# Kernel optimization log

Measured on AMD Instinct MI355X. Metric: run time of the kernel, lower is better.

## Reference

```python
import jax, jax.numpy as jnp
import numpy as np

N = 8192
H = 512
TAU = 0.8
LAM = 0.5
EPS = 1e-8


def setup_inputs() -> dict:
    key = jax.random.key(0)
    k1, k2, k3, k4, k5 = jax.random.split(key, 5)
    xavier_std = 1.414 * np.sqrt(2.0 / (H + H))  # xavier_normal_ with gain=1.414
    return {
        "z_mp": jax.random.normal(k1, (N, H), dtype=jnp.float32),
        "z_sc": jax.random.normal(k2, (N, H), dtype=jnp.float32),
        "pos": jax.random.randint(k3, (N, N), 0, 2, dtype=jnp.int32),
        "W1": (jax.random.normal(k4, (H, H), dtype=jnp.float32) * xavier_std),
        "b1": jnp.zeros((H,), dtype=jnp.float32),
        "W2": (jax.random.normal(k5, (H, H), dtype=jnp.float32) * xavier_std),
        "b2": jnp.zeros((H,), dtype=jnp.float32),
    }


def _proj(z, W1, b1, W2, b2):
    # nn.Linear applies x @ W.T + b
    h = jax.nn.elu(z @ W1.T + b1)
    return h @ W2.T + b2


def _sim(z1, z2, tau):
    # exp(cosine_similarity / tau), computed as in the original:
    # dot(z1, z2.T) / (|z1| |z2|.T) / tau
    n1 = jnp.linalg.norm(z1, axis=-1, keepdims=True)  # [N,1]
    n2 = jnp.linalg.norm(z2, axis=-1, keepdims=True)  # [N,1]
    dot = z1 @ z2.T                                   # [N,N]
    return jnp.exp(dot / (n1 * n2.T) / tau)


def reference(z_mp, z_sc, pos, W1, b1, W2, b2):
    pos_f = pos.astype(jnp.float32)
    zp_mp = _proj(z_mp, W1, b1, W2, b2)
    zp_sc = _proj(z_sc, W1, b1, W2, b2)

    m_mp2sc = _sim(zp_mp, zp_sc, TAU)   # [N,N]
    m_sc2mp = m_mp2sc.T                 # [N,N]

    # row-normalize, masked log-mean (mp -> sc)
    s_mp = m_mp2sc / (jnp.sum(m_mp2sc, axis=1, keepdims=True) + EPS)
    lori_mp = -jnp.mean(jnp.log(jnp.sum(s_mp * pos_f, axis=-1)))

    # row-normalize, masked log-mean (sc -> mp)
    s_sc = m_sc2mp / (jnp.sum(m_sc2mp, axis=1, keepdims=True) + EPS)
    lori_sc = -jnp.mean(jnp.log(jnp.sum(s_sc * pos_f, axis=-1)))

    return LAM * lori_mp + (1.0 - LAM) * lori_sc
```

## Files before the change

kernel.cpp:

```cpp
#include <hip/hip_runtime.h>
#include <stdint.h>


#define NN 8192
#define HH 512
#define TAUF 0.8f
#define EPSF 1e-8f
#define NW (NN / 32)

typedef __attribute__((ext_vector_type(8))) short short8;
typedef __attribute__((ext_vector_type(4))) float f32x4;
typedef __attribute__((ext_vector_type(4))) int i32x4;
typedef __attribute__((ext_vector_type(4))) unsigned short u16x4;
typedef unsigned short u16;
typedef unsigned int u32;

typedef __attribute__((address_space(1))) void GV;
typedef __attribute__((address_space(3))) void LV;

__device__ __forceinline__ void g2l16(const void* g, void* l) {
  __builtin_amdgcn_global_load_lds((const GV*)g, (LV*)l, 16, 0, 0);
}

__device__ __forceinline__ u16 f2bf(float x) {
  u32 u = __builtin_bit_cast(u32, x);
  u = (u + 0x7fffu + ((u >> 16) & 1u)) >> 16;
  return (u16)u;
}

__global__ __launch_bounds__(256)
void pack_kernel(const int* __restrict__ pos, u32* __restrict__ P) {
  int gid = blockIdx.x * 256 + threadIdx.x;
  const int* src = pos + (size_t)gid * 32;
  u32 w = 0;
#pragma unroll
  for (int c = 0; c < 8; ++c) {
    i32x4 p = *(const i32x4*)(src + c * 4);
    w |= ((u32)p.x & 1u) << (c * 4);
    w |= ((u32)p.y & 1u) << (c * 4 + 1);
    w |= ((u32)p.z & 1u) << (c * 4 + 2);
    w |= ((u32)p.w & 1u) << (c * 4 + 3);
  }
  P[gid] = w;
}

__global__ void cast_kernel(const float* __restrict__ in, u16* __restrict__ out, int n) {
  int i = (blockIdx.x * 256 + threadIdx.x) * 8;
  if (i >= n) return;
  f32x4 a = *(const f32x4*)(in + i);
  f32x4 b = *(const f32x4*)(in + i + 4);
  u16 o[8];
  o[0] = f2bf(a.x); o[1] = f2bf(a.y); o[2] = f2bf(a.z); o[3] = f2bf(a.w);
  o[4] = f2bf(b.x); o[5] = f2bf(b.y); o[6] = f2bf(b.z); o[7] = f2bf(b.w);
  i32x4 v;
  v.x = (int)(o[0] | ((u32)o[1] << 16)); v.y = (int)(o[2] | ((u32)o[3] << 16));
  v.z = (int)(o[4] | ((u32)o[5] << 16)); v.w = (int)(o[6] | ((u32)o[7] << 16));
  *(i32x4*)(out + i) = v;
}

template <int EPI>
__global__ __launch_bounds__(256)
void gemm_proj(const u16* __restrict__ A1, const u16* __restrict__ A2,
               const u16* __restrict__ W, const float* __restrict__ bias,
               void* __restrict__ out1, void* __restrict__ out2) {
  __shared__ __align__(16) u16 As[128 * 32];
  __shared__ __align__(16) u16 Bs[128 * 32];
  const int tid = threadIdx.x;
  const int lane = tid & 63, w = tid >> 6;
  const int lo = lane & 15, quad = lane >> 4;
  const int wy = w >> 1, wx = w & 1;
  const u16* A; char* Out; int m0;
  if (blockIdx.y < 64) { A = A1; Out = (char*)out1; m0 = blockIdx.y * 128; }
  else                 { A = A2; Out = (char*)out2; m0 = (blockIdx.y - 64) * 128; }
  const int n0 = blockIdx.x * 128;
  const int srow = w * 16 + (lane >> 2);
  const int skel = (lane & 3) * 8;
  char* AsB = (char*)As; char* BsB = (char*)Bs;
  f32x4 acc[4][4] = {};

  for (int k0 = 0; k0 < HH; k0 += 32) {
    const u16* ga = A + (size_t)(m0 + srow) * HH + k0 + skel;
    const u16* gb = W + (size_t)(n0 + srow) * HH + k0 + skel;
    g2l16(ga, AsB + w * 1024);
    g2l16(ga + (size_t)64 * HH, AsB + w * 1024 + 4096);
    g2l16(gb, BsB + w * 1024);
    g2l16(gb + (size_t)64 * HH, BsB + w * 1024 + 4096);
    asm volatile("s_waitcnt vmcnt(0)" ::: "memory");
    __syncthreads();
    short8 aF[4], bF[4];
#pragma unroll
    for (int mi = 0; mi < 4; ++mi)
      aF[mi] = *(const short8*)(AsB + (wy * 64 + mi * 16 + lo) * 64 + quad * 16);
#pragma unroll
    for (int ni = 0; ni < 4; ++ni)
      bF[ni] = *(const short8*)(BsB + (wx * 64 + ni * 16 + lo) * 64 + quad * 16);
#pragma unroll
    for (int mi = 0; mi < 4; ++mi)
#pragma unroll
      for (int ni = 0; ni < 4; ++ni)
        acc[mi][ni] = __builtin_amdgcn_mfma_f32_16x16x32_bf16(aF[mi], bF[ni], acc[mi][ni], 0, 0, 0);
    __syncthreads();
  }
#pragma unroll
  for (int mi = 0; mi < 4; ++mi) {
    int rl = wy * 64 + mi * 16 + quad * 4;
#pragma unroll
    for (int ni = 0; ni < 4; ++ni) {
      int cl = wx * 64 + ni * 16 + lo;
      float bv = bias[n0 + cl];
#pragma unroll
      for (int r = 0; r < 4; ++r) {
        float v = acc[mi][ni][r] + bv;
        size_t idx = (size_t)(m0 + rl + r) * HH + (n0 + cl);
        if (EPI == 0) {
          if (v < 0.f) v = __expf(v) - 1.f;
          ((u16*)Out)[idx] = f2bf(v);
        } else {
          ((float*)Out)[idx] = v;
        }
      }
    }
  }
}

__global__ void norm_kernel(const float* __restrict__ zp, u16* __restrict__ out, float scale) {
  const int row = blockIdx.x;
  const int t = threadIdx.x;
  const float* src = zp + (size_t)row * HH;
  f32x4 v = *(const f32x4*)(src + t * 4);
  float ss = v.x * v.x + v.y * v.y + v.z * v.z + v.w * v.w;
#pragma unroll
  for (int d = 1; d < 64; d <<= 1) ss += __shfl_xor(ss, d, 64);
  __shared__ float red[2];
  if ((t & 63) == 0) red[t >> 6] = ss;
  __syncthreads();
  float inv = scale * rsqrtf(red[0] + red[1]);
  u16x4 o;
  o[0] = f2bf(v.x * inv); o[1] = f2bf(v.y * inv);
  o[2] = f2bf(v.z * inv); o[3] = f2bf(v.w * inv);
  *(u16x4*)(out + (size_t)row * HH + t * 4) = o;
}

__global__ __launch_bounds__(256)
void sim_kernel(const u16* __restrict__ Az, const u16* __restrict__ Bz,
                const u32* __restrict__ Pbits,
                float* __restrict__ rowpart, float* __restrict__ posrowpart,
                float* __restrict__ colpart, float* __restrict__ poscolpart) {
  __shared__ __align__(16) u16 As[128 * 32];
  __shared__ __align__(16) u16 Bs[128 * 32];
  __shared__ u32 PBi[128 * 4];
  __shared__ u32 PBj[128 * 4];
  const int tid = threadIdx.x;
  const int lane = tid & 63, w = tid >> 6;
  const int lo = lane & 15, quad = lane >> 4;
  const int wy = w >> 1, wx = w & 1;

  const int bid = blockIdx.x + (int)gridDim.x * blockIdx.y;
  const int xcd = bid & 7, s = bid >> 3;
  const int by = xcd * 8 + (s >> 6);
  const int bx = s & 63;
  const int i0 = by * 128, j0 = bx * 128;

  const int srow = w * 16 + (lane >> 2);
  const int skel = (lane & 3) * 8;
  char* AsB = (char*)As; char* BsB = (char*)Bs;
  f32x4 acc[4][4] = {};

  for (int k0 = 0; k0 < HH; k0 += 32) {
    const u16* ga = Az + (size_t)(i0 + srow) * HH + k0 + skel;
    const u16* gb = Bz + (size_t)(j0 + srow) * HH + k0 + skel;
    g2l16(ga, AsB + w * 1024);
    g2l16(ga + (size_t)64 * HH, AsB + w * 1024 + 4096);
    g2l16(gb, BsB + w * 1024);
    g2l16(gb + (size_t)64 * HH, BsB + w * 1024 + 4096);
    asm volatile("s_waitcnt vmcnt(0)" ::: "memory");
    __syncthreads();
    short8 aF[4], bF[4];
#pragma unroll
    for (int mi = 0; mi < 4; ++mi)
      aF[mi] = *(const short8*)(AsB + (wy * 64 + mi * 16 + lo) * 64 + quad * 16);
#pragma unroll
    for (int ni = 0; ni < 4; ++ni)
      bF[ni] = *(const short8*)(BsB + (wx * 64 + ni * 16 + lo) * 64 + quad * 16);
#pragma unroll
    for (int mi = 0; mi < 4; ++mi)
#pragma unroll
      for (int ni = 0; ni < 4; ++ni)
        acc[mi][ni] = __builtin_amdgcn_mfma_f32_16x16x32_bf16(aF[mi], bF[ni], acc[mi][ni], 0, 0, 0);
    __syncthreads();
  }

  {
    int il = tid >> 1, w2 = (tid & 1) * 2;
    u32 a0 = Pbits[(size_t)(i0 + il) * NW + (j0 >> 5) + w2];
    u32 a1 = Pbits[(size_t)(i0 + il) * NW + (j0 >> 5) + w2 + 1];
    u32 b0 = Pbits[(size_t)(j0 + il) * NW + (i0 >> 5) + w2];
    u32 b1 = Pbits[(size_t)(j0 + il) * NW + (i0 >> 5) + w2 + 1];
    PBi[il * 4 + w2] = a0; PBi[il * 4 + w2 + 1] = a1;
    PBj[il * 4 + w2] = b0; PBj[il * 4 + w2 + 1] = b1;
  }

#pragma unroll
  for (int mi = 0; mi < 4; ++mi)
#pragma unroll
    for (int ni = 0; ni < 4; ++ni)
#pragma unroll
      for (int r = 0; r < 4; ++r)
        acc[mi][ni][r] = __expf(acc[mi][ni][r]);

  __syncthreads();

  const int rowb = wy * 64 + quad * 4;
  const int colb = wx * 64 + lo;

#pragma unroll
  for (int mi = 0; mi < 4; ++mi) {
    int rl = rowb + mi * 16;
    float rs[4], pr[4];
#pragma unroll
    for (int r = 0; r < 4; ++r) {
      u32 W0 = PBi[(rl + r) * 4 + wx * 2];
      u32 W1 = PBi[(rl + r) * 4 + wx * 2 + 1];
      float e0 = acc[mi][0][r], e1 = acc[mi][1][r];
      float e2 = acc[mi][2][r], e3 = acc[mi][3][r];
      rs[r] = (e0 + e1) + (e2 + e3);
      pr[r] = (((W0 >> lo) & 1u) ? e0 : 0.f) + (((W0 >> (16 + lo)) & 1u) ? e1 : 0.f) +
              (((W1 >> lo) & 1u) ? e2 : 0.f) + (((W1 >> (16 + lo)) & 1u) ? e3 : 0.f);
    }
#pragma unroll
    for (int d = 1; d < 16; d <<= 1) {
#pragma unroll
      for (int r = 0; r < 4; ++r) {
        rs[r] += __shfl_xor(rs[r], d, 64);
        pr[r] += __shfl_xor(pr[r], d, 64);
      }
    }
    if (lo == 0) {
      float* rp = rowpart + (size_t)(bx * 2 + wx) * NN;
      float* pp = posrowpart + (size_t)(bx * 2 + wx) * NN;
#pragma unroll
      for (int r = 0; r < 4; ++r) {
        rp[i0 + rl + r] = rs[r];
        pp[i0 + rl + r] = pr[r];
      }
    }
  }

#pragma unroll
  for (int ni = 0; ni < 4; ++ni) {
    int cl = colb + ni * 16;
    u32 W0 = PBj[cl * 4 + wy * 2];
    u32 W1 = PBj[cl * 4 + wy * 2 + 1];
    float cs = 0.f, pc = 0.f;
#pragma unroll
    for (int mi = 0; mi < 4; ++mi) {
      u32 W = (mi < 2) ? W0 : W1;
      int sh = (mi & 1) * 16 + quad * 4;
#pragma unroll
      for (int r = 0; r < 4; ++r) {
        float e = acc[mi][ni][r];
        cs += e;
        pc += ((W >> (sh + r)) & 1u) ? e : 0.f;
      }
    }
    cs += __shfl_xor(cs, 16, 64); cs += __shfl_xor(cs, 32, 64);
    pc += __shfl_xor(pc, 16, 64); pc += __shfl_xor(pc, 32, 64);
    if (quad == 0) {
      colpart[(size_t)(by * 2 + wy) * NN + j0 + cl] = cs;
      poscolpart[(size_t)(by * 2 + wy) * NN + j0 + cl] = pc;
    }
  }
}

__global__ __launch_bounds__(256)
void reduce1_kernel(const float* __restrict__ rowpart, const float* __restrict__ posrowpart,
                    const float* __restrict__ colpart, const float* __restrict__ poscolpart,
                    float* __restrict__ red) {
  int t = threadIdx.x;
  int i = blockIdx.x * 128 + (t >> 1);
  int half = t & 1;
  float rs = 0.f, pr = 0.f, cs = 0.f, pc = 0.f;
  for (int s = half * 64; s < half * 64 + 64; ++s) {
    rs += rowpart[(size_t)s * NN + i];
    pr += posrowpart[(size_t)s * NN + i];
    cs += colpart[(size_t)s * NN + i];
    pc += poscolpart[(size_t)s * NN + i];
  }
  rs += __shfl_xor(rs, 1, 64); pr += __shfl_xor(pr, 1, 64);
  cs += __shfl_xor(cs, 1, 64); pc += __shfl_xor(pc, 1, 64);
  float term = (half == 0) ? (__logf(pr / (rs + EPSF)) + __logf(pc / (cs + EPSF))) : 0.f;
#pragma unroll
  for (int d = 2; d < 64; d <<= 1) term += __shfl_xor(term, d, 64);
  __shared__ float rsh[4];
  if ((t & 63) == 0) rsh[t >> 6] = term;
  __syncthreads();
  if (t == 0) red[blockIdx.x] = rsh[0] + rsh[1] + rsh[2] + rsh[3];
}

__global__ void reduce2_kernel(const float* __restrict__ red, float* __restrict__ out) {
  float s = red[threadIdx.x];
#pragma unroll
  for (int d = 1; d < 64; d <<= 1) s += __shfl_xor(s, d, 64);
  if (threadIdx.x == 0) out[0] = -0.5f * s / (float)NN;
}

extern "C" void kernel_launch(void* const* d_in, const int* in_sizes, int n_in,
                              void* d_out, int out_size, void* d_ws, size_t ws_size,
                              hipStream_t stream) {
  const float* z_mp = (const float*)d_in[0];
  const float* z_sc = (const float*)d_in[1];
  const int* pos = (const int*)d_in[2];
  const float* W1 = (const float*)d_in[3];
  const float* b1 = (const float*)d_in[4];
  const float* W2 = (const float*)d_in[5];
  const float* b2 = (const float*)d_in[6];
  float* out = (float*)d_out;

  char* ws = (char*)d_ws;
  u32* Pbits = (u32*)(ws);
  u16* zbA = (u16*)(ws + 8388608);
  u16* zbB = (u16*)(ws + 16777216);
  u16* W1b = (u16*)(ws + 25165824);
  u16* W2b = (u16*)(ws + 25690112);
  u16* hA  = (u16*)(ws + 26214400);
  u16* hB  = (u16*)(ws + 34603008);
  float* zpA = (float*)(ws + 42991616);
  float* zpB = (float*)(ws + 59768832);
  u16* znA = zbA;
  u16* znB = zbB;
  float* rowpart    = (float*)(ws + 26214400);
  float* posrowpart = (float*)(ws + 30408704);
  float* colpart    = (float*)(ws + 34603008);
  float* poscolpart = (float*)(ws + 38797312);
  float* red64 = (float*)(ws + 76546048);

  pack_kernel<<<NN * NW / 256, 256, 0, stream>>>(pos, Pbits);

  cast_kernel<<<2048, 256, 0, stream>>>(z_mp, zbA, NN * HH);
  cast_kernel<<<2048, 256, 0, stream>>>(z_sc, zbB, NN * HH);
  cast_kernel<<<128, 256, 0, stream>>>(W1, W1b, HH * HH);
  cast_kernel<<<128, 256, 0, stream>>>(W2, W2b, HH * HH);

  dim3 gp(4, 128);
  gemm_proj<0><<<gp, 256, 0, stream>>>(zbA, zbB, W1b, b1, hA, hB);
  gemm_proj<1><<<gp, 256, 0, stream>>>(hA, hB, W2b, b2, zpA, zpB);

  norm_kernel<<<NN, 128, 0, stream>>>(zpA, znA, 1.0f / TAUF);
  norm_kernel<<<NN, 128, 0, stream>>>(zpB, znB, 1.0f);

  dim3 gs(64, 64);
  sim_kernel<<<gs, 256, 0, stream>>>(znA, znB, Pbits, rowpart, posrowpart, colpart, poscolpart);
  reduce1_kernel<<<64, 256, 0, stream>>>(rowpart, posrowpart, colpart, poscolpart, red64);
  reduce2_kernel<<<1, 64, 0, stream>>>(red64, out);
}
```

Measured before the change: 586.8 us.

## Fuse prep and norm launches, deepen sim K-tile to 64, prefetch pos bits

The pack kernel and four cast kernels are merged into one prep launch, and the two norm launches become one. In the similarity kernel the K step grows from 32 to 64, so there are half as many loads and barriers per tile. The positive-mask bit loads are issued before the GEMM loop so their latency overlaps the main loop. The larger LDS tiles use more shared memory and more registers, which may reduce occupancy.

```diff
diff --git a/kernel.cpp b/kernel.cpp
--- a/kernel.cpp
+++ b/kernel.cpp
@@ -28,25 +28,7 @@
   return (u16)u;
 }
 
-__global__ __launch_bounds__(256)
-void pack_kernel(const int* __restrict__ pos, u32* __restrict__ P) {
-  int gid = blockIdx.x * 256 + threadIdx.x;
-  const int* src = pos + (size_t)gid * 32;
-  u32 w = 0;
-#pragma unroll
-  for (int c = 0; c < 8; ++c) {
-    i32x4 p = *(const i32x4*)(src + c * 4);
-    w |= ((u32)p.x & 1u) << (c * 4);
-    w |= ((u32)p.y & 1u) << (c * 4 + 1);
-    w |= ((u32)p.z & 1u) << (c * 4 + 2);
-    w |= ((u32)p.w & 1u) << (c * 4 + 3);
-  }
-  P[gid] = w;
-}
-
-__global__ void cast_kernel(const float* __restrict__ in, u16* __restrict__ out, int n) {
-  int i = (blockIdx.x * 256 + threadIdx.x) * 8;
-  if (i >= n) return;
+__device__ __forceinline__ void cast8(const float* __restrict__ in, u16* __restrict__ out, int i) {
   f32x4 a = *(const f32x4*)(in + i);
   f32x4 b = *(const f32x4*)(in + i + 4);
   u16 o[8];
@@ -56,6 +38,37 @@
   v.x = (int)(o[0] | ((u32)o[1] << 16)); v.y = (int)(o[2] | ((u32)o[3] << 16));
   v.z = (int)(o[4] | ((u32)o[5] << 16)); v.w = (int)(o[6] | ((u32)o[7] << 16));
   *(i32x4*)(out + i) = v;
+}
+
+__global__ __launch_bounds__(256)
+void prep_kernel(const int* __restrict__ pos, u32* __restrict__ P,
+                 const float* __restrict__ z_mp, u16* __restrict__ zbA,
+                 const float* __restrict__ z_sc, u16* __restrict__ zbB,
+                 const float* __restrict__ W1, u16* __restrict__ W1b,
+                 const float* __restrict__ W2, u16* __restrict__ W2b) {
+  int b = blockIdx.x, tid = threadIdx.x;
+  if (b < 8192) {
+    int gid = b * 256 + tid;
+    const int* src = pos + (size_t)gid * 32;
+    u32 w = 0;
+#pragma unroll
+    for (int c = 0; c < 8; ++c) {
+      i32x4 p = *(const i32x4*)(src + c * 4);
+      w |= ((u32)p.x & 1u) << (c * 4);
+      w |= ((u32)p.y & 1u) << (c * 4 + 1);
+      w |= ((u32)p.z & 1u) << (c * 4 + 2);
+      w |= ((u32)p.w & 1u) << (c * 4 + 3);
+    }
+    P[gid] = w;
+  } else if (b < 10240) {
+    cast8(z_mp, zbA, ((b - 8192) * 256 + tid) * 8);
+  } else if (b < 12288) {
+    cast8(z_sc, zbB, ((b - 10240) * 256 + tid) * 8);
+  } else if (b < 12416) {
+    cast8(W1, W1b, ((b - 12288) * 256 + tid) * 8);
+  } else {
+    cast8(W2, W2b, ((b - 12416) * 256 + tid) * 8);
+  }
 }
 
 template <int EPI>
@@ -123,10 +136,14 @@
   }
 }
 
-__global__ void norm_kernel(const float* __restrict__ zp, u16* __restrict__ out, float scale) {
-  const int row = blockIdx.x;
+__global__ void norm_kernel(const float* __restrict__ zpA, u16* __restrict__ znA,
+                            const float* __restrict__ zpB, u16* __restrict__ znB) {
+  const int row = blockIdx.x & (NN - 1);
+  const bool isA = blockIdx.x < NN;
+  const float* src = (isA ? zpA : zpB) + (size_t)row * HH;
+  u16* dst = (isA ? znA : znB) + (size_t)row * HH;
+  const float scale = isA ? (1.0f / TAUF) : 1.0f;
   const int t = threadIdx.x;
-  const float* src = zp + (size_t)row * HH;
   f32x4 v = *(const f32x4*)(src + t * 4);
   float ss = v.x * v.x + v.y * v.y + v.z * v.z + v.w * v.w;
 #pragma unroll
@@ -138,7 +155,7 @@
   u16x4 o;
   o[0] = f2bf(v.x * inv); o[1] = f2bf(v.y * inv);
   o[2] = f2bf(v.z * inv); o[3] = f2bf(v.w * inv);
-  *(u16x4*)(out + (size_t)row * HH + t * 4) = o;
+  *(u16x4*)(dst + t * 4) = o;
 }
 
 __global__ __launch_bounds__(256)
@@ -146,8 +163,8 @@
                 const u32* __restrict__ Pbits,
                 float* __restrict__ rowpart, float* __restrict__ posrowpart,
                 float* __restrict__ colpart, float* __restrict__ poscolpart) {
-  __shared__ __align__(16) u16 As[128 * 32];
-  __shared__ __align__(16) u16 Bs[128 * 32];
+  __shared__ __align__(16) u16 As[128 * 64];
+  __shared__ __align__(16) u16 Bs[128 * 64];
   __shared__ u32 PBi[128 * 4];
   __shared__ u32 PBj[128 * 4];
   const int tid = threadIdx.x;
@@ -161,44 +178,49 @@
   const int bx = s & 63;
   const int i0 = by * 128, j0 = bx * 128;
 
-  const int srow = w * 16 + (lane >> 2);
-  const int skel = (lane & 3) * 8;
+  const int il = tid >> 1, w2 = (tid & 1) * 2;
+  const u32* PiSrc = Pbits + (size_t)(i0 + il) * NW + (j0 >> 5) + w2;
+  const u32* PjSrc = Pbits + (size_t)(j0 + il) * NW + (i0 >> 5) + w2;
+  u32 pa0 = PiSrc[0], pa1 = PiSrc[1], pb0 = PjSrc[0], pb1 = PjSrc[1];
+
+  const int srow = lane >> 3;
+  const int skel = (lane & 7) * 8;
   char* AsB = (char*)As; char* BsB = (char*)Bs;
   f32x4 acc[4][4] = {};
 
-  for (int k0 = 0; k0 < HH; k0 += 32) {
-    const u16* ga = Az + (size_t)(i0 + srow) * HH + k0 + skel;
-    const u16* gb = Bz + (size_t)(j0 + srow) * HH + k0 + skel;
-    g2l16(ga, AsB + w * 1024);
-    g2l16(ga + (size_t)64 * HH, AsB + w * 1024 + 4096);
-    g2l16(gb, BsB + w * 1024);
-    g2l16(gb + (size_t)64 * HH, BsB + w * 1024 + 4096);
+  for (int k0 = 0; k0 < HH; k0 += 64) {
+    const u16* ga = Az + (size_t)(i0 + w * 32 + srow) * HH + k0 + skel;
+    const u16* gb = Bz + (size_t)(j0 + w * 32 + srow) * HH + k0 + skel;
+#pragma unroll
+    for (int t = 0; t < 4; ++t) {
+      g2l16(ga + (size_t)(t * 8) * HH, AsB + w * 4096 + t * 1024);
+      g2l16(gb + (size_t)(t * 8) * HH, BsB + w * 4096 + t * 1024);
+    }
     asm volatile("s_waitcnt vmcnt(0)" ::: "memory");
     __syncthreads();
-    short8 aF[4], bF[4];
+    short8 aF[4][2], bF[4][2];
 #pragma unroll
     for (int mi = 0; mi < 4; ++mi)
-      aF[mi] = *(const short8*)(AsB + (wy * 64 + mi * 16 + lo) * 64 + quad * 16);
+#pragma unroll
+      for (int ks = 0; ks < 2; ++ks)
+        aF[mi][ks] = *(const short8*)(AsB + (wy * 64 + mi * 16 + lo) * 128 + ks * 64 + quad * 16);
 #pragma unroll
     for (int ni = 0; ni < 4; ++ni)
-      bF[ni] = *(const short8*)(BsB + (wx * 64 + ni * 16 + lo) * 64 + quad * 16);
-#pragma unroll
-    for (int mi = 0; mi < 4; ++mi)
-#pragma unroll
-      for (int ni = 0; ni < 4; ++ni)
-        acc[mi][ni] = __builtin_amdgcn_mfma_f32_16x16x32_bf16(aF[mi], bF[ni], acc[mi][ni], 0, 0, 0);
+#pragma unroll
+      for (int ks = 0; ks < 2; ++ks)
+        bF[ni][ks] = *(const short8*)(BsB + (wx * 64 + ni * 16 + lo) * 128 + ks * 64 + quad * 16);
+#pragma unroll
+    for (int ks = 0; ks < 2; ++ks)
+#pragma unroll
+      for (int mi = 0; mi < 4; ++mi)
+#pragma unroll
+        for (int ni = 0; ni < 4; ++ni)
+          acc[mi][ni] = __builtin_amdgcn_mfma_f32_16x16x32_bf16(aF[mi][ks], bF[ni][ks], acc[mi][ni], 0, 0, 0);
     __syncthreads();
   }
 
-  {
-    int il = tid >> 1, w2 = (tid & 1) * 2;
-    u32 a0 = Pbits[(size_t)(i0 + il) * NW + (j0 >> 5) + w2];
-    u32 a1 = Pbits[(size_t)(i0 + il) * NW + (j0 >> 5) + w2 + 1];
-    u32 b0 = Pbits[(size_t)(j0 + il) * NW + (i0 >> 5) + w2];
-    u32 b1 = Pbits[(size_t)(j0 + il) * NW + (i0 >> 5) + w2 + 1];
-    PBi[il * 4 + w2] = a0; PBi[il * 4 + w2 + 1] = a1;
-    PBj[il * 4 + w2] = b0; PBj[il * 4 + w2 + 1] = b1;
-  }
+  PBi[il * 4 + w2] = pa0; PBi[il * 4 + w2 + 1] = pa1;
+  PBj[il * 4 + w2] = pb0; PBj[il * 4 + w2 + 1] = pb1;
 
 #pragma unroll
   for (int mi = 0; mi < 4; ++mi)
@@ -334,19 +356,13 @@
   float* poscolpart = (float*)(ws + 38797312);
   float* red64 = (float*)(ws + 76546048);
 
-  pack_kernel<<<NN * NW / 256, 256, 0, stream>>>(pos, Pbits);
-
-  cast_kernel<<<2048, 256, 0, stream>>>(z_mp, zbA, NN * HH);
-  cast_kernel<<<2048, 256, 0, stream>>>(z_sc, zbB, NN * HH);
-  cast_kernel<<<128, 256, 0, stream>>>(W1, W1b, HH * HH);
-  cast_kernel<<<128, 256, 0, stream>>>(W2, W2b, HH * HH);
+  prep_kernel<<<12544, 256, 0, stream>>>(pos, Pbits, z_mp, zbA, z_sc, zbB, W1, W1b, W2, W2b);
 
   dim3 gp(4, 128);
   gemm_proj<0><<<gp, 256, 0, stream>>>(zbA, zbB, W1b, b1, hA, hB);
   gemm_proj<1><<<gp, 256, 0, stream>>>(hA, hB, W2b, b2, zpA, zpB);
 
-  norm_kernel<<<NN, 128, 0, stream>>>(zpA, znA, 1.0f / TAUF);
-  norm_kernel<<<NN, 128, 0, stream>>>(zpB, znB, 1.0f);
+  norm_kernel<<<2 * NN, 128, 0, stream>>>(zpA, znA, zpB, znB);
 
   dim3 gs(64, 64);
   sim_kernel<<<gs, 256, 0, stream>>>(znA, znB, Pbits, rowpart, posrowpart, colpart, poscolpart);
```

Result: no change. 584.6 us (-0.4%).
